# Optimization experiments

Measured on AMD Instinct MI355X. Metric: run time of the kernel, lower is better.

## Reference

```python
import jax, jax.numpy as jnp
import numpy as np

N = 100000        # num_nodes
W_IN = 256        # input feature dim
W_OUT = 64        # args.node_dim
C = 2             # args.num_channels
T = 4             # num_edge_type
E = 800000        # edges per edge type
NUM_CLASS = 4
M = 20000         # number of target nodes
BETA = 0.5        # args.beta


def setup_inputs() -> dict:
    key = jax.random.key(0)
    ks = jax.random.split(key, 10)
    X = jax.random.normal(ks[0], (N, W_IN), dtype=jnp.float32)
    edge_index = jax.random.randint(ks[1], (T, 2, E), 0, N)
    edge_value = jax.random.uniform(ks[2], (T, E), dtype=jnp.float32)
    target_x = jax.random.randint(ks[3], (M,), 0, N)
    target = jax.random.randint(ks[4], (M,), 0, NUM_CLASS)
    # learned params
    Ws = jax.random.normal(ks[5], (C, W_IN, W_OUT), dtype=jnp.float32) * 0.05   # GCNConv weights
    conv_weight = jax.random.normal(ks[6], (C, T), dtype=jnp.float32) * 0.1     # FastGTConv.weight
    linear1_W = jax.random.normal(ks[7], (W_OUT, W_OUT * C), dtype=jnp.float32) * 0.05
    linear1_b = jnp.zeros((W_OUT,), dtype=jnp.float32)
    lin_W = jax.random.normal(ks[8], (NUM_CLASS, W_OUT), dtype=jnp.float32) * 0.05
    lin_b = jnp.zeros((NUM_CLASS,), dtype=jnp.float32)
    return dict(X=X, edge_value=edge_value, Ws=Ws, conv_weight=conv_weight,
                linear1_W=linear1_W, linear1_b=linear1_b, lin_W=lin_W, lin_b=lin_b,
                edge_index=edge_index, target_x=target_x, target=target)


def reference(X, edge_value, Ws, conv_weight, linear1_W, linear1_b, lin_W, lin_b,
              edge_index, target_x, target):
    # FastGTConv: softmax over edge types per channel
    filt = jax.nn.softmax(conv_weight, axis=1)            # [C, T]
    rows = edge_index[:, 0, :].reshape(-1)                # [T*E]
    cols = edge_index[:, 1, :].reshape(-1)                # [T*E]
    # X_ = H = [X @ W_c for each channel]
    X_ = jnp.einsum('nd,cdo->cno', X, Ws)                 # [C, N, W_OUT]
    outs = []
    for c in range(C):
        # concat+coalesce(add) then spmm == scatter-add of weighted messages
        vals = (edge_value * filt[c][:, None]).reshape(-1)       # [T*E]
        msgs = vals[:, None] * X_[c][cols]                        # [T*E, W_OUT]
        Hc = jax.ops.segment_sum(msgs, rows, num_segments=N)      # [N, W_OUT]
        outs.append(jax.nn.relu(BETA * X_[c] + (1.0 - BETA) * Hc))
    H_ = jnp.concatenate(outs, axis=1)                    # [N, C*W_OUT]
    H_ = jax.nn.relu(H_ @ linear1_W.T + linear1_b)        # [N, W_OUT]
    y = H_[target_x] @ lin_W.T + lin_b                    # [M, NUM_CLASS]
    logp = jax.nn.log_softmax(y, axis=-1)
    loss = -jnp.mean(jnp.take_along_axis(logp, target[:, None], axis=1))
    return loss, y
```

## Files before the change

### kernel.cpp

```cpp
#include <hip/hip_runtime.h>

#define N_NODES 100000
#define W_INF   256
#define W_OUTF  64
#define C_CH    2
#define T_ET    4
#define E_EDGE  800000
#define NUM_CLS 4
#define M_TGT   20000
#define BETA    0.5f
#define MAXDEG  96

typedef __attribute__((ext_vector_type(8))) short bf16x8;
typedef __attribute__((ext_vector_type(4))) float floatx4;

__device__ inline short f2bf(float f) {
    unsigned u = __builtin_bit_cast(unsigned, f);
    u += 0x7FFF + ((u >> 16) & 1);
    return (short)(u >> 16);
}
__device__ inline float bflo(unsigned q) { return __builtin_bit_cast(float, q << 16); }
__device__ inline float bfhi(unsigned q) { return __builtin_bit_cast(float, q & 0xFFFF0000u); }

__global__ void setup_kernel(const float* __restrict__ Ws,
                             const float* __restrict__ conv_weight,
                             const int* __restrict__ target_x,
                             short* __restrict__ Bt, float* __restrict__ filt,
                             int* __restrict__ rid, int* __restrict__ nrows,
                             float* __restrict__ out) {
    int i = blockIdx.x * 256 + threadIdx.x;
    if (i == 0) { *nrows = 0; out[0] = 0.f; }
    if (i < C_CH) {
        int c = i;
        float mx = -1e30f;
        for (int t = 0; t < T_ET; t++) mx = fmaxf(mx, conv_weight[c * T_ET + t]);
        float e[T_ET];
        float s = 0.f;
        for (int t = 0; t < T_ET; t++) { e[t] = expf(conv_weight[c * T_ET + t] - mx); s += e[t]; }
        for (int t = 0; t < T_ET; t++) filt[c * T_ET + t] = e[t] / s;
    }
    if (i < C_CH * W_OUTF * W_INF) {
        int co = i >> 8, k = i & 255;
        int c = co >> 6, o = co & 63;
        Bt[i] = f2bf(Ws[((size_t)c * W_INF + k) * W_OUTF + o]);
    }
    if (i < M_TGT) rid[target_x[i]] = -2;
}

__global__ void compact_kernel(int* __restrict__ rid, int* __restrict__ row_list,
                               int* __restrict__ nrows, int* __restrict__ counts) {
    int n = blockIdx.x * blockDim.x + threadIdx.x;
    if (n < M_TGT) counts[n] = 0;
    int lane = threadIdx.x & 63;
    bool flag = (n < N_NODES) && (rid[n] == -2);
    unsigned long long mask = __ballot(flag);
    int base = 0;
    if (lane == 0 && mask) base = atomicAdd(nrows, __popcll(mask));
    base = __shfl(base, 0);
    if (flag) {
        int id = base + __popcll(mask & ((1ULL << lane) - 1ULL));
        rid[n] = id;
        row_list[id] = n;
    }
}

#define GMT  64
#define BLDA 264
#define GEMM_NB  ((N_NODES + GMT - 1) / GMT)
#define BUILD_BX ((E_EDGE / 8 + 255) / 256)
__global__ __launch_bounds__(256, 4)
void fused_gemm_build(const float* __restrict__ X, const short* __restrict__ Bt,
                      short* __restrict__ Xp,
                      const int* __restrict__ edge_index,
                      const float* __restrict__ edge_value,
                      const int* __restrict__ rid,
                      int* __restrict__ counts,
                      unsigned long long* __restrict__ records) {
    __shared__ short Bl[64][BLDA];
    int tid = threadIdx.x;
    if (blockIdx.x < GEMM_NB) {
        int w = tid >> 6, lane = tid & 63;
        int quad = lane >> 4, l15 = lane & 15;
        int m0 = blockIdx.x * GMT + w * 16;
        int arow = m0 + l15;
        if (arow >= N_NODES) arow = N_NODES - 1;
        const float* xrow = X + (size_t)arow * W_INF;
        bf16x8 af[8];
        #pragma unroll
        for (int kc = 0; kc < 8; kc++) {
            int kb = kc * 32 + quad * 8;
            float4 v0 = *(const float4*)&xrow[kb];
            float4 v1 = *(const float4*)&xrow[kb + 4];
            af[kc][0] = f2bf(v0.x); af[kc][1] = f2bf(v0.y);
            af[kc][2] = f2bf(v0.z); af[kc][3] = f2bf(v0.w);
            af[kc][4] = f2bf(v1.x); af[kc][5] = f2bf(v1.y);
            af[kc][6] = f2bf(v1.z); af[kc][7] = f2bf(v1.w);
        }
        floatx4 acc[C_CH][4] = {};
        for (int c = 0; c < C_CH; c++) {
            if (c) __syncthreads();
            #pragma unroll
            for (int l = 0; l < 8; l++) {
                int idx = tid + l * 256;
                int r = idx >> 5;
                int kp = (idx & 31) * 8;
                *(bf16x8*)&Bl[r][kp] = *(const bf16x8*)&Bt[(size_t)(c * 64 + r) * W_INF + kp];
            }
            __syncthreads();
            #pragma unroll
            for (int kc = 0; kc < 8; kc++) {
                int kb = kc * 32 + quad * 8;
                #pragma unroll
                for (int nt = 0; nt < 4; nt++) {
                    bf16x8 b = *(bf16x8*)&Bl[nt * 16 + l15][kb];
                    acc[c][nt] = __builtin_amdgcn_mfma_f32_16x16x32_bf16(af[kc], b, acc[c][nt], 0, 0, 0);
                }
            }
        }
        #pragma unroll
        for (int nt = 0; nt < 4; nt++) {
            int o = nt * 16 + l15;
            #pragma unroll
            for (int r = 0; r < 4; r++) {
                int m = m0 + quad * 4 + r;
                if (m < N_NODES) {
                    unsigned pk = (unsigned)(unsigned short)f2bf(acc[0][nt][r])
                                | ((unsigned)(unsigned short)f2bf(acc[1][nt][r]) << 16);
                    *(unsigned*)&Xp[(size_t)m * (C_CH * W_OUTF) + o * 2] = pk;
                }
            }
        }
    } else {
        int bb = blockIdx.x - GEMM_NB;
        int t = bb / BUILD_BX;
        int i = (bb - t * BUILD_BX) * 256 + tid;
        if (i >= E_EDGE / 8) return;
        int e = i * 8;
        const int*   rbase = &edge_index[(size_t)(t * 2 + 0) * E_EDGE + e];
        const int*   cbase = &edge_index[(size_t)(t * 2 + 1) * E_EDGE + e];
        const float* vbase = &edge_value[(size_t)t * E_EDGE + e];
        int4   r4a = *(const int4*)  &rbase[0], r4b = *(const int4*)  &rbase[4];
        int4   c4a = *(const int4*)  &cbase[0], c4b = *(const int4*)  &cbase[4];
        float4 v4a = *(const float4*)&vbase[0], v4b = *(const float4*)&vbase[4];
        int rows[8] = {r4a.x, r4a.y, r4a.z, r4a.w, r4b.x, r4b.y, r4b.z, r4b.w};
        int cols[8] = {c4a.x, c4a.y, c4a.z, c4a.w, c4b.x, c4b.y, c4b.z, c4b.w};
        float evv[8] = {v4a.x, v4a.y, v4a.z, v4a.w, v4b.x, v4b.y, v4b.z, v4b.w};
        int ids[8];
        #pragma unroll
        for (int j = 0; j < 8; j++) ids[j] = rid[rows[j]];
        #pragma unroll
        for (int j = 0; j < 8; j++) {
            if (ids[j] >= 0) {
                int p = atomicAdd(&counts[ids[j]], 1);
                if (p < MAXDEG) {
                    unsigned long long rec =
                        (unsigned long long)(unsigned)(cols[j] | (t << 20)) |
                        ((unsigned long long)__float_as_uint(evv[j]) << 32);
                    records[(size_t)ids[j] * MAXDEG + p] = rec;
                }
            }
        }
    }
}

__global__ void gather_kernel(const int* __restrict__ row_list,
                              const int* __restrict__ counts,
                              const unsigned long long* __restrict__ records,
                              const float* __restrict__ filt,
                              const short* __restrict__ Xp,
                              float* __restrict__ Hcat,
                              const int* __restrict__ nrows_ptr) {
    int w = threadIdx.x >> 6, lane = threadIdx.x & 63;
    int b = blockIdx.x * 4 + w;
    if (b >= *nrows_ptr) return;
    float f0[T_ET], f1[T_ET];
    #pragma unroll
    for (int t = 0; t < T_ET; t++) { f0[t] = filt[t]; f1[t] = filt[T_ET + t]; }
    int n = row_list[b];
    int cnt = counts[b]; if (cnt > MAXDEG) cnt = MAXDEG;
    const unsigned long long* rec = records + (size_t)b * MAXDEG;
    const unsigned* xb = (const unsigned*)Xp + lane;
    float a0 = 0.f, a1 = 0.f;
    int p = 0;
    for (; p + 3 < cnt; p += 4) {
        unsigned long long r0 = rec[p],     r1 = rec[p + 1];
        unsigned long long r2 = rec[p + 2], r3 = rec[p + 3];
        int k0 = (int)(unsigned)r0, k1 = (int)(unsigned)r1;
        int k2 = (int)(unsigned)r2, k3 = (int)(unsigned)r3;
        float e0 = __uint_as_float((unsigned)(r0 >> 32));
        float e1 = __uint_as_float((unsigned)(r1 >> 32));
        float e2 = __uint_as_float((unsigned)(r2 >> 32));
        float e3 = __uint_as_float((unsigned)(r3 >> 32));
        unsigned q0 = xb[(size_t)(k0 & 0xFFFFF) * 64];
        unsigned q1 = xb[(size_t)(k1 & 0xFFFFF) * 64];
        unsigned q2 = xb[(size_t)(k2 & 0xFFFFF) * 64];
        unsigned q3 = xb[(size_t)(k3 & 0xFFFFF) * 64];
        int t0 = k0 >> 20, t1 = k1 >> 20, t2 = k2 >> 20, t3 = k3 >> 20;
        a0 += e0 * f0[t0] * bflo(q0) + e1 * f0[t1] * bflo(q1)
            + e2 * f0[t2] * bflo(q2) + e3 * f0[t3] * bflo(q3);
        a1 += e0 * f1[t0] * bfhi(q0) + e1 * f1[t1] * bfhi(q1)
            + e2 * f1[t2] * bfhi(q2) + e3 * f1[t3] * bfhi(q3);
    }
    for (; p < cnt; p++) {
        unsigned long long r0 = rec[p];
        int k0 = (int)(unsigned)r0;
        float e0 = __uint_as_float((unsigned)(r0 >> 32));
        unsigned q0 = xb[(size_t)(k0 & 0xFFFFF) * 64];
        int t0 = k0 >> 20;
        a0 += e0 * f0[t0] * bflo(q0);
        a1 += e0 * f1[t0] * bfhi(q0);
    }
    unsigned qn = xb[(size_t)n * 64];
    float h0 = BETA * bflo(qn) + (1.f - BETA) * a0;
    float h1 = BETA * bfhi(qn) + (1.f - BETA) * a1;
    Hcat[(size_t)b * (C_CH * W_OUTF) + lane]          = fmaxf(h0, 0.f);
    Hcat[(size_t)b * (C_CH * W_OUTF) + W_OUTF + lane] = fmaxf(h1, 0.f);
}

#define HTGT 16
__global__ void head_kernel(const float* __restrict__ Hcat,
                            const int* __restrict__ rid,
                            const float* __restrict__ W1,
                            const float* __restrict__ b1,
                            const float* __restrict__ linW,
                            const float* __restrict__ linb,
                            const int* __restrict__ target_x,
                            const int* __restrict__ target,
                            float* __restrict__ out) {
    __shared__ float w1s[C_CH * W_OUTF][W_OUTF + 1];
    __shared__ float hcat_s[4][C_CH * W_OUTF];
    __shared__ float loss_s[4];
    int tid = threadIdx.x;
    for (int i = tid; i < W_OUTF * C_CH * W_OUTF; i += 256) {
        int o = i >> 7, k = i & 127;
        w1s[k][o] = W1[i];
    }
    int wave = tid >> 6, lane = tid & 63;
    float l0 = linW[0 * W_OUTF + lane], l1 = linW[1 * W_OUTF + lane];
    float l2 = linW[2 * W_OUTF + lane], l3 = linW[3 * W_OUTF + lane];
    float lb0 = linb[0], lb1 = linb[1], lb2 = linb[2], lb3 = linb[3];
    float bias = b1[lane];
    float lsum = 0.f;
    __syncthreads();
    for (int it = 0; it < HTGT / 4; it++) {
        int m = blockIdx.x * HTGT + it * 4 + wave;
        int row = target_x[m];
        int id = rid[row];
        hcat_s[wave][lane]      = Hcat[(size_t)id * (C_CH * W_OUTF) + lane];
        hcat_s[wave][64 + lane] = Hcat[(size_t)id * (C_CH * W_OUTF) + 64 + lane];
        __syncthreads();
        float acc = bias;
        #pragma unroll 8
        for (int k = 0; k < C_CH * W_OUTF; k++) acc += hcat_s[wave][k] * w1s[k][lane];
        float h2 = fmaxf(acc, 0.f);
        float p0 = l0 * h2, p1 = l1 * h2, p2 = l2 * h2, p3 = l3 * h2;
        #pragma unroll
        for (int off = 32; off > 0; off >>= 1) {
            p0 += __shfl_xor(p0, off);
            p1 += __shfl_xor(p1, off);
            p2 += __shfl_xor(p2, off);
            p3 += __shfl_xor(p3, off);
        }
        if (lane == 0) {
            float y[NUM_CLS];
            y[0] = p0 + lb0; y[1] = p1 + lb1; y[2] = p2 + lb2; y[3] = p3 + lb3;
            float mx = fmaxf(fmaxf(y[0], y[1]), fmaxf(y[2], y[3]));
            float s = 0.f;
            #pragma unroll
            for (int k = 0; k < NUM_CLS; k++) s += expf(y[k] - mx);
            float lse = mx + logf(s);
            #pragma unroll
            for (int k = 0; k < NUM_CLS; k++) out[1 + (size_t)m * NUM_CLS + k] = y[k];
            int tg = target[m];
            lsum += lse - y[tg];
        }
        __syncthreads();
    }
    if (lane == 0) loss_s[wave] = lsum;
    __syncthreads();
    if (tid == 0) {
        float L = loss_s[0] + loss_s[1] + loss_s[2] + loss_s[3];
        atomicAdd(&out[0], L * (1.0f / (float)M_TGT));
    }
}

extern "C" void kernel_launch(void* const* d_in, const int* in_sizes, int n_in,
                              void* d_out, int out_size, void* d_ws, size_t ws_size,
                              hipStream_t stream) {
    const float* X           = (const float*)d_in[0];
    const float* edge_value  = (const float*)d_in[1];
    const float* Ws          = (const float*)d_in[2];
    const float* conv_weight = (const float*)d_in[3];
    const float* linear1_W   = (const float*)d_in[4];
    const float* linear1_b   = (const float*)d_in[5];
    const float* lin_W       = (const float*)d_in[6];
    const float* lin_b       = (const float*)d_in[7];
    const int*   edge_index  = (const int*)d_in[8];
    const int*   target_x    = (const int*)d_in[9];
    const int*   target      = (const int*)d_in[10];
    float* out = (float*)d_out;

    char* ws = (char*)d_ws;
    size_t off = 0;
    float* filt  = (float*)(ws + off); off += 256;
    size_t xbytes = (size_t)N_NODES * C_CH * W_OUTF * sizeof(short);
    short* Xp    = (short*)(ws + off); off += xbytes;
    float* Hcat  = (float*)(ws + off); off += (size_t)M_TGT * C_CH * W_OUTF * sizeof(float);
    unsigned long long* records = (unsigned long long*)(ws + off);
    off += (size_t)M_TGT * MAXDEG * sizeof(unsigned long long);
    short* Bt    = (short*)(ws + off); off += (size_t)C_CH * W_OUTF * W_INF * sizeof(short);
    int*   rid   = (int*)  (ws + off); off += (size_t)N_NODES * sizeof(int);
    int*   row_list = (int*)(ws + off); off += (size_t)M_TGT * sizeof(int);
    int*   counts   = (int*)(ws + off); off += (size_t)M_TGT * sizeof(int);
    int*   nrows    = (int*)(ws + off); off += 256;

    hipMemsetAsync(rid, 0xFF, (size_t)N_NODES * sizeof(int), stream);

    setup_kernel<<<128, 256, 0, stream>>>(Ws, conv_weight, target_x, Bt, filt, rid, nrows, out);
    compact_kernel<<<(N_NODES + 255) / 256, 256, 0, stream>>>(rid, row_list, nrows, counts);
    fused_gemm_build<<<GEMM_NB + BUILD_BX * T_ET, 256, 0, stream>>>(
        X, Bt, Xp, edge_index, edge_value, rid, counts, records);
    gather_kernel<<<(M_TGT + 3) / 4, 256, 0, stream>>>(row_list, counts, records, filt, Xp, Hcat, nrows);
    head_kernel<<<M_TGT / HTGT, 256, 0, stream>>>(Hcat, rid, linear1_W, linear1_b, lin_W, lin_b,
                                                  target_x, target, out);
}
```

Baseline: 313.6 us.

## Interleave GEMM and edge-build blocks, halve LDS tile, deepen gather unroll

The fused GEMM/build kernel now interleaves GEMM and edge-build blocks by block-index parity, so both kinds of work run side by side on the GPU instead of all GEMM blocks being scheduled first. The B tile in shared memory is halved by loading it in four 32-row chunks, and launch bounds are raised to 6 blocks per CU to increase occupancy. The gather loop gains an 8-wide unrolled path that issues all record loads and feature loads before accumulating, to expose more memory-level parallelism. The extra syncthreads and chunked B loads add some overhead, and the grid is sized as twice the build block count, which assumes that count covers every GEMM block.

```diff
diff --git a/kernel.cpp b/kernel.cpp
--- a/kernel.cpp
+++ b/kernel.cpp
@@ -68,7 +68,8 @@
 #define BLDA 264
 #define GEMM_NB  ((N_NODES + GMT - 1) / GMT)
 #define BUILD_BX ((E_EDGE / 8 + 255) / 256)
-__global__ __launch_bounds__(256, 4)
+#define BUILD_TOT (BUILD_BX * T_ET)
+__global__ __launch_bounds__(256, 6)
 void fused_gemm_build(const float* __restrict__ X, const short* __restrict__ Bt,
                       short* __restrict__ Xp,
                       const int* __restrict__ edge_index,
@@ -76,12 +77,15 @@
                       const int* __restrict__ rid,
                       int* __restrict__ counts,
                       unsigned long long* __restrict__ records) {
-    __shared__ short Bl[64][BLDA];
+    __shared__ short Bl[32][BLDA];
     int tid = threadIdx.x;
-    if (blockIdx.x < GEMM_NB) {
+    int bx = blockIdx.x;
+    if ((bx & 1) == 0) {
+        int g = bx >> 1;
+        if (g >= GEMM_NB) return;
         int w = tid >> 6, lane = tid & 63;
         int quad = lane >> 4, l15 = lane & 15;
-        int m0 = blockIdx.x * GMT + w * 16;
+        int m0 = g * GMT + w * 16;
         int arow = m0 + l15;
         if (arow >= N_NODES) arow = N_NODES - 1;
         const float* xrow = X + (size_t)arow * W_INF;
@@ -97,41 +101,45 @@
             af[kc][6] = f2bf(v1.z); af[kc][7] = f2bf(v1.w);
         }
         floatx4 acc[C_CH][4] = {};
-        for (int c = 0; c < C_CH; c++) {
-            if (c) __syncthreads();
-            #pragma unroll
-            for (int l = 0; l < 8; l++) {
+        #pragma unroll 1
+        for (int ch = 0; ch < 4; ch++) {
+            int c = ch >> 1, h = ch & 1;
+            if (ch) __syncthreads();
+            #pragma unroll
+            for (int l = 0; l < 4; l++) {
                 int idx = tid + l * 256;
                 int r = idx >> 5;
                 int kp = (idx & 31) * 8;
-                *(bf16x8*)&Bl[r][kp] = *(const bf16x8*)&Bt[(size_t)(c * 64 + r) * W_INF + kp];
+                *(bf16x8*)&Bl[r][kp] =
+                    *(const bf16x8*)&Bt[(size_t)(c * 64 + h * 32 + r) * W_INF + kp];
             }
             __syncthreads();
             #pragma unroll
             for (int kc = 0; kc < 8; kc++) {
                 int kb = kc * 32 + quad * 8;
                 #pragma unroll
-                for (int nt = 0; nt < 4; nt++) {
+                for (int nt = 0; nt < 2; nt++) {
                     bf16x8 b = *(bf16x8*)&Bl[nt * 16 + l15][kb];
-                    acc[c][nt] = __builtin_amdgcn_mfma_f32_16x16x32_bf16(af[kc], b, acc[c][nt], 0, 0, 0);
+                    acc[c][h * 2 + nt] =
+                        __builtin_amdgcn_mfma_f32_16x16x32_bf16(af[kc], b, acc[c][h * 2 + nt], 0, 0, 0);
                 }
             }
         }
         #pragma unroll
-        for (int nt = 0; nt < 4; nt++) {
-            int o = nt * 16 + l15;
+        for (int j = 0; j < 4; j++) {
+            int o = (j >> 1) * 32 + (j & 1) * 16 + l15;
             #pragma unroll
             for (int r = 0; r < 4; r++) {
                 int m = m0 + quad * 4 + r;
                 if (m < N_NODES) {
-                    unsigned pk = (unsigned)(unsigned short)f2bf(acc[0][nt][r])
-                                | ((unsigned)(unsigned short)f2bf(acc[1][nt][r]) << 16);
+                    unsigned pk = (unsigned)(unsigned short)f2bf(acc[0][j][r])
+                                | ((unsigned)(unsigned short)f2bf(acc[1][j][r]) << 16);
                     *(unsigned*)&Xp[(size_t)m * (C_CH * W_OUTF) + o * 2] = pk;
                 }
             }
         }
     } else {
-        int bb = blockIdx.x - GEMM_NB;
+        int bb = bx >> 1;
         int t = bb / BUILD_BX;
         int i = (bb - t * BUILD_BX) * 256 + tid;
         if (i >= E_EDGE / 8) return;
@@ -182,24 +190,34 @@
     const unsigned* xb = (const unsigned*)Xp + lane;
     float a0 = 0.f, a1 = 0.f;
     int p = 0;
+    for (; p + 7 < cnt; p += 8) {
+        unsigned long long rr[8];
+        #pragma unroll
+        for (int j = 0; j < 8; j++) rr[j] = rec[p + j];
+        unsigned q[8];
+        #pragma unroll
+        for (int j = 0; j < 8; j++)
+            q[j] = xb[(size_t)((unsigned)rr[j] & 0xFFFFF) * 64];
+        #pragma unroll
+        for (int j = 0; j < 8; j++) {
+            int t = (int)((unsigned)rr[j] >> 20);
+            float e = __uint_as_float((unsigned)(rr[j] >> 32));
+            a0 += e * f0[t] * bflo(q[j]);
+            a1 += e * f1[t] * bfhi(q[j]);
+        }
+    }
     for (; p + 3 < cnt; p += 4) {
-        unsigned long long r0 = rec[p],     r1 = rec[p + 1];
-        unsigned long long r2 = rec[p + 2], r3 = rec[p + 3];
-        int k0 = (int)(unsigned)r0, k1 = (int)(unsigned)r1;
-        int k2 = (int)(unsigned)r2, k3 = (int)(unsigned)r3;
-        float e0 = __uint_as_float((unsigned)(r0 >> 32));
-        float e1 = __uint_as_float((unsigned)(r1 >> 32));
-        float e2 = __uint_as_float((unsigned)(r2 >> 32));
-        float e3 = __uint_as_float((unsigned)(r3 >> 32));
-        unsigned q0 = xb[(size_t)(k0 & 0xFFFFF) * 64];
-        unsigned q1 = xb[(size_t)(k1 & 0xFFFFF) * 64];
-        unsigned q2 = xb[(size_t)(k2 & 0xFFFFF) * 64];
-        unsigned q3 = xb[(size_t)(k3 & 0xFFFFF) * 64];
-        int t0 = k0 >> 20, t1 = k1 >> 20, t2 = k2 >> 20, t3 = k3 >> 20;
-        a0 += e0 * f0[t0] * bflo(q0) + e1 * f0[t1] * bflo(q1)
-            + e2 * f0[t2] * bflo(q2) + e3 * f0[t3] * bflo(q3);
-        a1 += e0 * f1[t0] * bfhi(q0) + e1 * f1[t1] * bfhi(q1)
-            + e2 * f1[t2] * bfhi(q2) + e3 * f1[t3] * bfhi(q3);
+        unsigned long long rr[4];
+        #pragma unroll
+        for (int j = 0; j < 4; j++) rr[j] = rec[p + j];
+        #pragma unroll
+        for (int j = 0; j < 4; j++) {
+            unsigned q = xb[(size_t)((unsigned)rr[j] & 0xFFFFF) * 64];
+            int t = (int)((unsigned)rr[j] >> 20);
+            float e = __uint_as_float((unsigned)(rr[j] >> 32));
+            a0 += e * f0[t] * bflo(q);
+            a1 += e * f1[t] * bfhi(q);
+        }
     }
     for (; p < cnt; p++) {
         unsigned long long r0 = rec[p];
@@ -318,7 +336,7 @@
 
     setup_kernel<<<128, 256, 0, stream>>>(Ws, conv_weight, target_x, Bt, filt, rid, nrows, out);
     compact_kernel<<<(N_NODES + 255) / 256, 256, 0, stream>>>(rid, row_list, nrows, counts);
-    fused_gemm_build<<<GEMM_NB + BUILD_BX * T_ET, 256, 0, stream>>>(
+    fused_gemm_build<<<2 * BUILD_TOT, 256, 0, stream>>>(
         X, Bt, Xp, edge_index, edge_value, rid, counts, records);
     gather_kernel<<<(M_TGT + 3) / 4, 256, 0, stream>>>(row_list, counts, records, filt, Xp, Hcat, nrows);
     head_kernel<<<M_TGT / HTGT, 256, 0, stream>>>(Hcat, rid, linear1_W, linear1_b, lin_W, lin_b,
```

After: 352.0 us. 1.12x slower.
